# Kernel tuning notes

Hardware: AMD Instinct MI355X
Metric: run time of the kernel (lower is better)

The kernel has to match this reference:

```python
import jax, jax.numpy as jnp
import numpy as np

B, N, C, H = 2, 1024, 768, 12
D = C // H  # head_dim = 64
LN_EPS = 1e-5
BN_EPS = 1e-5


def setup_inputs() -> dict:
    key = jax.random.key(0)
    ks = jax.random.split(key, 8)
    s = 0.02
    return {
        "x": jax.random.normal(ks[0], (B, N, C), jnp.float32),
        "qkv_w": jax.random.normal(ks[1], (3 * C, C), jnp.float32) * s,
        "qkv_b": jnp.zeros((3 * C,), jnp.float32),
        "ln_g": jnp.ones((3 * C,), jnp.float32),
        "ln_b": jnp.zeros((3 * C,), jnp.float32),
        "scale": jnp.float32(D ** -0.5),
        "riem_scale": jnp.float32(D ** -0.5),
        "temp": jnp.ones((2 * H, 1, 1), jnp.float32),
        "bn_g": jnp.ones((2 * H,), jnp.float32),
        "bn_b": jnp.zeros((2 * H,), jnp.float32),
        "bn_mean": jnp.zeros((2 * H,), jnp.float32),
        "bn_var": jnp.ones((2 * H,), jnp.float32),
        "conv_w": jax.random.normal(ks[2], (H, 2 * H), jnp.float32) * s,  # 1x1 conv: [out_ch, in_ch]
        "conv_b": jnp.zeros((H,), jnp.float32),
        "proj_w": jax.random.normal(ks[3], (C, C), jnp.float32) * s,
        "proj_b": jnp.zeros((C,), jnp.float32),
    }


def _layernorm(x, g, b):
    mu = jnp.mean(x, axis=-1, keepdims=True)
    var = jnp.mean((x - mu) ** 2, axis=-1, keepdims=True)
    return (x - mu) * jax.lax.rsqrt(var + LN_EPS) * g + b


def reference(x, qkv_w, qkv_b, ln_g, ln_b, scale, riem_scale, temp,
              bn_g, bn_b, bn_mean, bn_var, conv_w, conv_b, proj_w, proj_b):
    Bq, Nq, Cq = x.shape
    qkv = _layernorm(x @ qkv_w.T + qkv_b, ln_g, ln_b)            # [B,N,3C]
    qkv = qkv.reshape(Bq, Nq, 3, H, D).transpose(2, 0, 3, 1, 4)  # [3,B,H,N,D]
    q, k, v = qkv[0], qkv[1], qkv[2]

    qk = jnp.einsum('bhid,bhjd->bhij', q, k)                     # shared QK^T GEMM
    attn = qk * scale
    # cov Frobenius: ||q_i q_i^T - k_j k_j^T||_F = sqrt(|q|^4 + |k|^4 - 2 (q.k)^2)
    qn2 = jnp.sum(q * q, axis=-1)                                # [B,H,N]
    kn2 = jnp.sum(k * k, axis=-1)
    frob2 = qn2[..., :, None] ** 2 + kn2[..., None, :] ** 2 - 2.0 * qk * qk
    attn_r = jnp.sqrt(jnp.maximum(frob2, 1e-12)) * riem_scale

    a = jnp.concatenate([attn, attn_r], axis=1) * temp[None]     # [B,2H,N,N]
    # BatchNorm2d (eval mode, running stats)
    inv = jax.lax.rsqrt(bn_var + BN_EPS)
    a = (a - bn_mean[None, :, None, None]) * (inv * bn_g)[None, :, None, None] + bn_b[None, :, None, None]
    # 1x1 conv: channel mixing 2H -> H
    a = jnp.einsum('bcij,oc->boij', a, conv_w) + conv_b[None, :, None, None]
    a = jax.nn.softmax(a, axis=-1)                               # [B,H,N,N]

    out = jnp.einsum('bhij,bhjd->bhid', a, v)                    # [B,H,N,D]
    out = out.transpose(0, 2, 1, 3).reshape(Bq, Nq, Cq)
    return out @ proj_w.T + proj_b
```

## Files before the change

### kernel.cpp

```cpp
#include <hip/hip_runtime.h>
#include <stdint.h>
#include <string.h>


using short8  = __attribute__((ext_vector_type(8))) short;
using float4v = __attribute__((ext_vector_type(4))) float;
using uint2v  = __attribute__((ext_vector_type(2))) unsigned int;
typedef unsigned short u16;

__device__ __forceinline__ float bf2f(u16 u) {
  uint32_t x = ((uint32_t)u) << 16; float f; __builtin_memcpy(&f, &x, 4); return f;
}
__device__ __forceinline__ u16 f2bf(float f) {
  uint32_t x; __builtin_memcpy(&x, &f, 4);
  uint32_t r = x + 0x7FFFu + ((x >> 16) & 1u);
  return (u16)(r >> 16);
}
__device__ __forceinline__ float gets(const void* p, int i, bool f32) {
  return f32 ? ((const float*)p)[i] : bf2f(((const u16*)p)[i]);
}
__device__ __forceinline__ void gl_lds(const void* g, void* l) {
  __builtin_amdgcn_global_load_lds(
      (const __attribute__((address_space(1))) void*)g,
      (__attribute__((address_space(3))) void*)l, 16, 0, 0);
}

#define CN0 (2048 * 768)
#define CN1 (2304 * 768)
#define CN2 (2304)
#define CN3 (768 * 768)
#define CN4 (768)
#define CTOT (CN0 + CN1 + CN2 + CN3 + CN4)

__launch_bounds__(256)
__global__ void cast_all(const void* __restrict__ s0, const void* __restrict__ s1,
                         const void* __restrict__ s2, const void* __restrict__ s3,
                         const void* __restrict__ s4, u16* __restrict__ dst,
                         const u16* __restrict__ lng) {
  const bool f32 = (lng[0] == 0);
  const int i8 = (blockIdx.x * 256 + threadIdx.x) * 8;
  if (i8 >= CTOT) return;
  const void* src; int off;
  if (i8 < CN0)                         { src = s0; off = i8; }
  else if (i8 < CN0 + CN1)              { src = s1; off = i8 - CN0; }
  else if (i8 < CN0 + CN1 + CN2)        { src = s2; off = i8 - CN0 - CN1; }
  else if (i8 < CN0 + CN1 + CN2 + CN3)  { src = s3; off = i8 - CN0 - CN1 - CN2; }
  else                                  { src = s4; off = i8 - CN0 - CN1 - CN2 - CN3; }
  short8 v;
  if (f32) {
    const float4v a = *reinterpret_cast<const float4v*>((const float*)src + off);
    const float4v b = *reinterpret_cast<const float4v*>((const float*)src + off + 4);
#pragma unroll
    for (int j = 0; j < 4; j++) { v[j] = (short)f2bf(a[j]); v[j + 4] = (short)f2bf(b[j]); }
  } else {
    v = *reinterpret_cast<const short8*>((const u16*)src + off);
  }
  *reinterpret_cast<short8*>(dst + i8) = v;
}

template<int BM, int BN>
__launch_bounds__(256, 4)
__global__ void gemm_lds(const u16* __restrict__ A, const u16* __restrict__ Bw,
                         const u16* __restrict__ bias, void* __restrict__ out,
                         const u16* __restrict__ lng, int M, int Nn, int K, int out_mode) {
  __shared__ u16 As[BM * 32], Bs[BN * 32];
  constexpr int FM = BM / 32, FN = BN / 32;
  const bool f32 = (lng[0] == 0);
  const int t = threadIdx.x, lane = t & 63, wave = t >> 6;
  const int quad = lane >> 4, l16 = lane & 15;
  const int m0 = blockIdx.y * BM, n0 = blockIdx.x * BN;
  const int wm = (wave & 1) * (BM / 2), wn = (wave >> 1) * (BN / 2);
  const int srow = wave * 16 + (lane >> 2), scol = (lane & 3) * 8;
  float4v acc[FM][FN] = {};
  for (int k0 = 0; k0 < K; k0 += 32) {
#pragma unroll
    for (int r = 0; r < BM; r += 64)
      gl_lds(A + (size_t)(m0 + r + srow) * K + k0 + scol, &As[(r + wave * 16) * 32]);
#pragma unroll
    for (int r = 0; r < BN; r += 64)
      gl_lds(Bw + (size_t)(n0 + r + srow) * K + k0 + scol, &Bs[(r + wave * 16) * 32]);
    __syncthreads();
    short8 af[FM], bfr[FN];
#pragma unroll
    for (int i = 0; i < FM; i++)
      af[i] = *reinterpret_cast<const short8*>(&As[(wm + i * 16 + l16) * 32 + quad * 8]);
#pragma unroll
    for (int i = 0; i < FN; i++)
      bfr[i] = *reinterpret_cast<const short8*>(&Bs[(wn + i * 16 + l16) * 32 + quad * 8]);
#pragma unroll
    for (int mi = 0; mi < FM; mi++)
#pragma unroll
      for (int ni = 0; ni < FN; ni++)
        acc[mi][ni] = __builtin_amdgcn_mfma_f32_16x16x32_bf16(af[mi], bfr[ni], acc[mi][ni], 0, 0, 0);
    __syncthreads();
  }
#pragma unroll
  for (int mi = 0; mi < FM; mi++) {
#pragma unroll
    for (int ni = 0; ni < FN; ni++) {
      const int col = n0 + wn + ni * 16 + l16;
      const float bv = bf2f(bias[col]);
#pragma unroll
      for (int r = 0; r < 4; r++) {
        const int row = m0 + wm + mi * 16 + quad * 4 + r;
        const float v = acc[mi][ni][r] + bv;
        const size_t idx = (size_t)row * Nn + col;
        if (out_mode == 0 || f32) ((float*)out)[idx] = v;
        else                      ((u16*)out)[idx] = f2bf(v);
      }
    }
  }
}

__launch_bounds__(256)
__global__ void ln_split(const float* __restrict__ raw, const void* __restrict__ g,
                         const void* __restrict__ b, u16* __restrict__ Q,
                         u16* __restrict__ Kk, u16* __restrict__ V,
                         float* __restrict__ qn4, float* __restrict__ kn4) {
  const bool f32 = (((const u16*)g)[0] == 0);
  const int row = blockIdx.x;
  const int bb = row >> 10, n = row & 1023;
  const int t = threadIdx.x, wave = t >> 6, lane = t & 63;
  const float* rp = raw + (size_t)row * 2304;
  float v[9], s1 = 0.f, s2 = 0.f;
#pragma unroll
  for (int k = 0; k < 9; k++) { float x = rp[t + 256 * k]; v[k] = x; s1 += x; s2 += x * x; }
#pragma unroll
  for (int m = 32; m >= 1; m >>= 1) { s1 += __shfl_xor(s1, m); s2 += __shfl_xor(s2, m); }
  __shared__ float r1[4], r2[4], hs[24];
  if (lane == 0) { r1[wave] = s1; r2[wave] = s2; }
  __syncthreads();
  const float S1 = r1[0] + r1[1] + r1[2] + r1[3];
  const float S2 = r2[0] + r2[1] + r2[2] + r2[3];
  const float mean = S1 * (1.f / 2304.f);
  const float var = S2 * (1.f / 2304.f) - mean * mean;
  const float rstd = rsqrtf(var + 1e-5f);
  float y[9];
#pragma unroll
  for (int k = 0; k < 9; k++) {
    const int c = t + 256 * k;
    y[k] = (v[k] - mean) * rstd * gets(g, c, f32) + gets(b, c, f32);
    const int s = k / 3;
    const int h = (k - s * 3) * 4 + wave, d = lane;
    const size_t idx = ((size_t)(bb * 12 + h) * 1024 + n) * 64 + d;
    u16* dst = (s == 0) ? Q : ((s == 1) ? Kk : V);
    dst[idx] = f2bf(y[k]);
  }
#pragma unroll
  for (int k = 0; k < 6; k++) {
    float sq = y[k] * y[k];
#pragma unroll
    for (int m = 32; m >= 1; m >>= 1) sq += __shfl_xor(sq, m);
    const int s = k / 3, h = (k - s * 3) * 4 + wave;
    if (lane == 0) hs[s * 12 + h] = sq;
  }
  __syncthreads();
  if (t < 12)      qn4[(size_t)(bb * 12 + t) * 1024 + n]      = hs[t] * hs[t];
  else if (t < 24) kn4[(size_t)(bb * 12 + t - 12) * 1024 + n] = hs[t] * hs[t];
}

__launch_bounds__(256)
__global__ void transpose_v(const u16* __restrict__ V, u16* __restrict__ Vt) {
  __shared__ u16 tile[64 * 65];
  const int bh = blockIdx.y;
  const int n0 = blockIdx.x * 64;
  const int t = threadIdx.x;
  const u16* src = V + (size_t)bh * 1024 * 64;
  u16* dst = Vt + (size_t)bh * 64 * 1024;
#pragma unroll
  for (int k = 0; k < 16; k++) {
    const int idx = t + 256 * k, n = idx >> 6, d = idx & 63;
    tile[d * 65 + n] = src[(size_t)(n0 + n) * 64 + d];
  }
  __syncthreads();
#pragma unroll
  for (int k = 0; k < 16; k++) {
    const int idx = t + 256 * k, d = idx >> 6, n = idx & 63;
    dst[(size_t)d * 1024 + n0 + n] = tile[d * 65 + n];
  }
}

__launch_bounds__(256)
__global__ void wp_setup(const void* __restrict__ scale_p, const void* __restrict__ riem_p,
                         const void* __restrict__ temp_p,
                         const void* __restrict__ bng, const void* __restrict__ bnb,
                         const void* __restrict__ bnm, const void* __restrict__ bnv,
                         const void* __restrict__ convw, const void* __restrict__ convb,
                         const u16* __restrict__ lng, float* __restrict__ Wp_g) {
  const bool f32 = (lng[0] == 0);
  const float LOG2E = 1.4426950408889634f;
  const int t = threadIdx.x;
  for (int idx = t; idx < 288; idx += 256) {
    const int o = idx / 24, c = idx % 24;
    const int co = (c & 1) ? 12 + (c >> 1) : (c >> 1);
    const float inv = rsqrtf(gets(bnv, co, f32) + 1e-5f);
    const float Ac = gets(temp_p, co, f32) * gets(bng, co, f32) * inv;
    const float sc = (co < 12) ? gets(scale_p, 0, f32) : gets(riem_p, 0, f32);
    Wp_g[c * 12 + o] = gets(convw, o * 24 + co, f32) * Ac * sc * LOG2E;
  }
  if (t < 12) {
    float sb = gets(convb, t, f32);
    for (int c = 0; c < 24; c++) {
      const float inv = rsqrtf(gets(bnv, c, f32) + 1e-5f);
      const float Bc = gets(bnb, c, f32) - gets(bnm, c, f32) * gets(bng, c, f32) * inv;
      sb += gets(convw, t * 24 + c, f32) * Bc;
    }
    Wp_g[24 * 12 + t] = sb * LOG2E;
  }
}

__launch_bounds__(256, 3)
__global__ void attn_fused(const u16* __restrict__ Q, const u16* __restrict__ Kk,
                           const u16* __restrict__ Vt,
                           const float* __restrict__ qn4, const float* __restrict__ kn4,
                           const float* __restrict__ Wp_g,
                           float* __restrict__ Pacc, float* __restrict__ Pl, int S) {
  __shared__ uint32_t Gd[512 * 17];
  __shared__ u16 P[12 * 648];

  const int t = threadIdx.x, lane = t & 63, wave = t >> 6;
  const int quad = lane >> 4, l16 = lane & 15;
  const int wg = blockIdx.x;
  const int bit = wg / S, s = wg - bit * S;
  const int jps = 32 / S;
  const int bb = bit >> 6, it = bit & 63, i0 = it * 16;

  for (int idx = t; idx < 512 * 4; idx += 256) {
    const int pos = idx >> 2, d = 12 + (idx & 3);
    Gd[pos * 17 + d] = (d == 12) ? 0x00003F80u : 0u;
  }

  short8 wfrag;
#pragma unroll
  for (int jj = 0; jj < 8; jj++) {
    const int c = quad * 8 + jj;
    wfrag[jj] = (short)f2bf((c < 25 && l16 < 12) ? Wp_g[c * 12 + l16] : 0.f);
  }

  const int hb = wave * 3;
  short8 aq[3][2];
  float qn4r[3][4];
#pragma unroll
  for (int hh = 0; hh < 3; hh++) {
    const int h = hb + hh;
    const u16* Qb = Q + ((size_t)(bb * 12 + h) * 1024 + i0 + l16) * 64;
#pragma unroll
    for (int ks = 0; ks < 2; ks++)
      aq[hh][ks] = *reinterpret_cast<const short8*>(Qb + ks * 32 + quad * 8);
#pragma unroll
    for (int r = 0; r < 4; r++)
      qn4r[hh][r] = qn4[(size_t)(bb * 12 + h) * 1024 + i0 + quad * 4 + r];
  }
  __syncthreads();

  float l_run[4] = {0.f, 0.f, 0.f, 0.f};
  float4v acc[3][4] = {};

  for (int jt = s * jps; jt < (s + 1) * jps; jt++) {
    const int j0 = jt * 32;
#pragma unroll
    for (int jc = 0; jc < 2; jc++) {
      float4v cc[3];
      float knr[3];
#pragma unroll
      for (int hh = 0; hh < 3; hh++) {
        const int h = hb + hh;
        knr[hh] = kn4[(size_t)(bb * 12 + h) * 1024 + j0 + jc * 16 + l16];
        const u16* Kr = Kk + ((size_t)(bb * 12 + h) * 1024 + j0 + jc * 16 + l16) * 64 + quad * 8;
        const short8 b0 = *reinterpret_cast<const short8*>(Kr);
        const short8 b1 = *reinterpret_cast<const short8*>(Kr + 32);
        float4v c = {};
        c = __builtin_amdgcn_mfma_f32_16x16x32_bf16(aq[hh][0], b0, c, 0, 0, 0);
        cc[hh] = __builtin_amdgcn_mfma_f32_16x16x32_bf16(aq[hh][1], b1, c, 0, 0, 0);
      }
#pragma unroll
      for (int hh = 0; hh < 3; hh++) {
#pragma unroll
        for (int r = 0; r < 4; r++) {
          const int pos = (quad * 4 + r) * 32 + jc * 16 + l16;
          const float qk = cc[hh][r];
          const float fr = qn4r[hh][r] + knr[hh] - 2.f * qk * qk;
          const float rv = sqrtf(fmaxf(fr, 1e-12f));
          Gd[pos * 17 + hb + hh] = (uint32_t)f2bf(qk) | ((uint32_t)f2bf(rv) << 16);
        }
      }
    }
    __syncthreads();

#pragma unroll
    for (int ir = 0; ir < 4; ir++) {
      const int i = wave * 4 + ir;
      short8 a0, a1;
      {
        const uint32_t* g0 = &Gd[(size_t)(i * 32 + l16) * 17 + quad * 4];
        uint32_t w0[4] = {g0[0], g0[1], g0[2], g0[3]};
        __builtin_memcpy(&a0, w0, 16);
        const uint32_t* g1 = &Gd[(size_t)(i * 32 + 16 + l16) * 17 + quad * 4];
        uint32_t w1[4] = {g1[0], g1[1], g1[2], g1[3]};
        __builtin_memcpy(&a1, w1, 16);
      }
      float4v L0 = {}, L1 = {};
      L0 = __builtin_amdgcn_mfma_f32_16x16x32_bf16(a0, wfrag, L0, 0, 0, 0);
      L1 = __builtin_amdgcn_mfma_f32_16x16x32_bf16(a1, wfrag, L1, 0, 0, 0);
      float ts = 0.f, p0[4], p1[4];
#pragma unroll
      for (int r = 0; r < 4; r++) {
        p0[r] = exp2f(L0[r]); p1[r] = exp2f(L1[r]);
        ts += p0[r] + p1[r];
      }
      ts += __shfl_xor(ts, 16);
      ts += __shfl_xor(ts, 32);
      l_run[ir] += ts;
      if (l16 < 12) {
        const uint2v w0 = { (uint32_t)f2bf(p0[0]) | ((uint32_t)f2bf(p0[1]) << 16),
                            (uint32_t)f2bf(p0[2]) | ((uint32_t)f2bf(p0[3]) << 16) };
        const uint2v w1 = { (uint32_t)f2bf(p1[0]) | ((uint32_t)f2bf(p1[1]) << 16),
                            (uint32_t)f2bf(p1[2]) | ((uint32_t)f2bf(p1[3]) << 16) };
        *reinterpret_cast<uint2v*>(&P[l16 * 648 + i * 40 + quad * 4]) = w0;
        *reinterpret_cast<uint2v*>(&P[l16 * 648 + i * 40 + 16 + quad * 4]) = w1;
      }
    }
    __syncthreads();

#pragma unroll
    for (int oo = 0; oo < 3; oo++) {
      const int o = hb + oo;
      const short8 pf = *reinterpret_cast<const short8*>(&P[o * 648 + l16 * 40 + quad * 8]);
      const u16* Vb = Vt + (size_t)(bb * 12 + o) * 64 * 1024;
#pragma unroll
      for (int ni = 0; ni < 4; ni++) {
        const short8 bv = *reinterpret_cast<const short8*>(Vb + (size_t)(ni * 16 + l16) * 1024 + j0 + quad * 8);
        acc[oo][ni] = __builtin_amdgcn_mfma_f32_16x16x32_bf16(pf, bv, acc[oo][ni], 0, 0, 0);
      }
    }
  }

#pragma unroll
  for (int ir = 0; ir < 4; ir++)
    if (l16 < 12 && quad == 0)
      Pl[(wg * 12 + l16) * 16 + wave * 4 + ir] = l_run[ir];
#pragma unroll
  for (int oo = 0; oo < 3; oo++) {
    const int o = hb + oo;
#pragma unroll
    for (int ni = 0; ni < 4; ni++)
#pragma unroll
      for (int r = 0; r < 4; r++) {
        const int i = quad * 4 + r, d = ni * 16 + l16;
        Pacc[((size_t)(wg * 12 + o) * 16 + i) * 64 + d] = acc[oo][ni][r];
      }
  }
}

__launch_bounds__(256)
__global__ void combine(const float* __restrict__ Pacc, const float* __restrict__ Pl,
                        u16* __restrict__ AO, int S) {
  const int o = blockIdx.x, bit = blockIdx.y;
  const int t = threadIdx.x, i = t >> 4, d0 = (t & 15) * 4;
  const int bb = bit >> 6, row = (bit & 63) * 16 + i;
  float lg = 0.f;
  float4v ov = {};
  for (int s2 = 0; s2 < S; s2++) {
    lg += Pl[((bit * S + s2) * 12 + o) * 16 + i];
    const float4v p = *reinterpret_cast<const float4v*>(
        Pacc + ((size_t)((bit * S + s2) * 12 + o) * 16 + i) * 64 + d0);
#pragma unroll
    for (int r = 0; r < 4; r++) ov[r] += p[r];
  }
  const float inv = 1.f / lg;
  uint2v pk;
  pk[0] = (uint32_t)f2bf(ov[0] * inv) | ((uint32_t)f2bf(ov[1] * inv) << 16);
  pk[1] = (uint32_t)f2bf(ov[2] * inv) | ((uint32_t)f2bf(ov[3] * inv) << 16);
  *reinterpret_cast<uint2v*>(&AO[((size_t)bb * 1024 + row) * 768 + o * 64 + d0]) = pk;
}

extern "C" void kernel_launch(void* const* d_in, const int* in_sizes, int n_in,
                              void* d_out, int out_size, void* d_ws, size_t ws_size,
                              hipStream_t stream) {
  const void* x      = d_in[0];
  const void* qkv_w  = d_in[1];
  const void* qkv_b  = d_in[2];
  const u16*  ln_g   = (const u16*)d_in[3];
  const void* ln_b   = d_in[4];
  const void* scale  = d_in[5];
  const void* riem   = d_in[6];
  const void* temp   = d_in[7];
  const void* bn_g   = d_in[8];
  const void* bn_b   = d_in[9];
  const void* bn_m   = d_in[10];
  const void* bn_v   = d_in[11];
  const void* conv_w = d_in[12];
  const void* conv_b = d_in[13];
  const void* proj_w = d_in[14];
  const void* proj_b = d_in[15];

  float* qkv_raw = (float*)d_ws;
  u16* Q   = (u16*)((char*)d_ws + (size_t)2048 * 2304 * 4);
  u16* Kk  = Q  + (size_t)2 * 12 * 1024 * 64;
  u16* V   = Kk + (size_t)2 * 12 * 1024 * 64;
  u16* Vt  = V  + (size_t)2 * 12 * 1024 * 64;
  float* qn4 = (float*)(Vt + (size_t)2 * 12 * 1024 * 64);
  float* kn4 = qn4 + 2 * 12 * 1024;
  u16* AO  = (u16*)(kn4 + 2 * 12 * 1024);
  u16* x_bf    = AO + (size_t)2048 * 768;
  u16* qkvw_bf = x_bf + CN0;
  u16* qkvb_bf = qkvw_bf + CN1;
  u16* projw_bf = qkvb_bf + CN2;
  u16* projb_bf = projw_bf + CN3;
  float* Wp_g = (float*)((char*)d_ws +
      (((size_t)(projb_bf + CN4) - (size_t)d_ws + 255) & ~(size_t)255));
  float* Pacc = (float*)((char*)Wp_g + ((300 * 4 + 255) & ~255));
  const size_t base_bytes = (size_t)((char*)Pacc - (char*)d_ws);

  int S = 8;
  while (S > 1 && base_bytes + (size_t)128 * S * 12 * 16 * 260 > ws_size) S >>= 1;
  float* Pl = Pacc + (size_t)128 * S * 12 * 16 * 64;

  cast_all<<<dim3((CTOT / 8 + 255) / 256), 256, 0, stream>>>(
      x, qkv_w, qkv_b, proj_w, proj_b, x_bf, ln_g);
  wp_setup<<<dim3(1), 256, 0, stream>>>(scale, riem, temp, bn_g, bn_b, bn_m, bn_v,
                                        conv_w, conv_b, ln_g, Wp_g);
  gemm_lds<64, 128><<<dim3(18, 32), 256, 0, stream>>>(x_bf, qkvw_bf, qkvb_bf, qkv_raw,
                                                      ln_g, 2048, 2304, 768, 0);
  ln_split<<<dim3(2048), 256, 0, stream>>>(qkv_raw, ln_g, ln_b, Q, Kk, V, qn4, kn4);
  transpose_v<<<dim3(16, 24), 256, 0, stream>>>(V, Vt);
  attn_fused<<<dim3(128 * S), 256, 0, stream>>>(Q, Kk, Vt, qn4, kn4, Wp_g, Pacc, Pl, S);
  combine<<<dim3(12, 128), 256, 0, stream>>>(Pacc, Pl, AO, S);
  gemm_lds<64, 64><<<dim3(12, 32), 256, 0, stream>>>(AO, projw_bf, projb_bf, d_out,
                                                     ln_g, 2048, 768, 768, 1);
}
```

Before: 233.6 us.

## Shrink intermediates to bf16, fuse weight setup, prefetch V, use hardware converts

Several changes at once. The QKV GEMM output and the attention partial accumulators are now stored as bf16 instead of fp32, which roughly halves that traffic. The wp_setup kernel is merged into cast_all to save a launch. V tiles are loaded into registers before the QK/softmax phase to hide their latency, and the split count is made a compile-time template parameter. Manual bf16 rounding and exp2f are replaced with hardware builtins where available. The cost is lower precision in the LayerNorm input and in the partial-sum reduction, plus extra register pressure from the V prefetch.

```diff
diff --git a/kernel.cpp b/kernel.cpp
--- a/kernel.cpp
+++ b/kernel.cpp
@@ -4,6 +4,7 @@
 
 
 using short8  = __attribute__((ext_vector_type(8))) short;
+using short4v = __attribute__((ext_vector_type(4))) short;
 using float4v = __attribute__((ext_vector_type(4))) float;
 using uint2v  = __attribute__((ext_vector_type(2))) unsigned int;
 typedef unsigned short u16;
@@ -16,6 +17,21 @@
   uint32_t r = x + 0x7FFFu + ((x >> 16) & 1u);
   return (u16)(r >> 16);
 }
+#if __has_builtin(__builtin_amdgcn_cvt_pk_bf16_f32)
+__device__ __forceinline__ uint32_t pk_bf16(float lo, float hi) {
+  auto r = __builtin_amdgcn_cvt_pk_bf16_f32(lo, hi);
+  uint32_t u; __builtin_memcpy(&u, &r, 4); return u;
+}
+#else
+__device__ __forceinline__ uint32_t pk_bf16(float lo, float hi) {
+  return (uint32_t)f2bf(lo) | ((uint32_t)f2bf(hi) << 16);
+}
+#endif
+#if __has_builtin(__builtin_amdgcn_exp2f)
+#define EXP2F __builtin_amdgcn_exp2f
+#else
+#define EXP2F exp2f
+#endif
 __device__ __forceinline__ float gets(const void* p, int i, bool f32) {
   return f32 ? ((const float*)p)[i] : bf2f(((const u16*)p)[i]);
 }
@@ -36,26 +52,53 @@
 __global__ void cast_all(const void* __restrict__ s0, const void* __restrict__ s1,
                          const void* __restrict__ s2, const void* __restrict__ s3,
                          const void* __restrict__ s4, u16* __restrict__ dst,
-                         const u16* __restrict__ lng) {
+                         const void* __restrict__ scale_p, const void* __restrict__ riem_p,
+                         const void* __restrict__ temp_p,
+                         const void* __restrict__ bng, const void* __restrict__ bnb,
+                         const void* __restrict__ bnm, const void* __restrict__ bnv,
+                         const void* __restrict__ convw, const void* __restrict__ convb,
+                         const u16* __restrict__ lng, float* __restrict__ Wp_g) {
   const bool f32 = (lng[0] == 0);
-  const int i8 = (blockIdx.x * 256 + threadIdx.x) * 8;
-  if (i8 >= CTOT) return;
-  const void* src; int off;
-  if (i8 < CN0)                         { src = s0; off = i8; }
-  else if (i8 < CN0 + CN1)              { src = s1; off = i8 - CN0; }
-  else if (i8 < CN0 + CN1 + CN2)        { src = s2; off = i8 - CN0 - CN1; }
-  else if (i8 < CN0 + CN1 + CN2 + CN3)  { src = s3; off = i8 - CN0 - CN1 - CN2; }
-  else                                  { src = s4; off = i8 - CN0 - CN1 - CN2 - CN3; }
-  short8 v;
-  if (f32) {
-    const float4v a = *reinterpret_cast<const float4v*>((const float*)src + off);
-    const float4v b = *reinterpret_cast<const float4v*>((const float*)src + off + 4);
-#pragma unroll
-    for (int j = 0; j < 4; j++) { v[j] = (short)f2bf(a[j]); v[j + 4] = (short)f2bf(b[j]); }
-  } else {
-    v = *reinterpret_cast<const short8*>((const u16*)src + off);
-  }
-  *reinterpret_cast<short8*>(dst + i8) = v;
+  const int t = threadIdx.x;
+  const int i8 = (blockIdx.x * 256 + t) * 8;
+  if (i8 < CTOT) {
+    const void* src; int off;
+    if (i8 < CN0)                         { src = s0; off = i8; }
+    else if (i8 < CN0 + CN1)              { src = s1; off = i8 - CN0; }
+    else if (i8 < CN0 + CN1 + CN2)        { src = s2; off = i8 - CN0 - CN1; }
+    else if (i8 < CN0 + CN1 + CN2 + CN3)  { src = s3; off = i8 - CN0 - CN1 - CN2; }
+    else                                  { src = s4; off = i8 - CN0 - CN1 - CN2 - CN3; }
+    short8 v;
+    if (f32) {
+      const float4v a = *reinterpret_cast<const float4v*>((const float*)src + off);
+      const float4v b = *reinterpret_cast<const float4v*>((const float*)src + off + 4);
+#pragma unroll
+      for (int j = 0; j < 4; j++) { v[j] = (short)f2bf(a[j]); v[j + 4] = (short)f2bf(b[j]); }
+    } else {
+      v = *reinterpret_cast<const short8*>((const u16*)src + off);
+    }
+    *reinterpret_cast<short8*>(dst + i8) = v;
+  }
+  if (blockIdx.x == 0) {
+    const float LOG2E = 1.4426950408889634f;
+    for (int idx = t; idx < 288; idx += 256) {
+      const int o = idx / 24, c = idx % 24;
+      const int co = (c & 1) ? 12 + (c >> 1) : (c >> 1);
+      const float inv = rsqrtf(gets(bnv, co, f32) + 1e-5f);
+      const float Ac = gets(temp_p, co, f32) * gets(bng, co, f32) * inv;
+      const float sc = (co < 12) ? gets(scale_p, 0, f32) : gets(riem_p, 0, f32);
+      Wp_g[c * 12 + o] = gets(convw, o * 24 + co, f32) * Ac * sc * LOG2E;
+    }
+    if (t < 12) {
+      float sb = gets(convb, t, f32);
+      for (int c = 0; c < 24; c++) {
+        const float inv = rsqrtf(gets(bnv, c, f32) + 1e-5f);
+        const float Bc = gets(bnb, c, f32) - gets(bnm, c, f32) * gets(bng, c, f32) * inv;
+        sb += gets(convw, t * 24 + c, f32) * Bc;
+      }
+      Wp_g[24 * 12 + t] = sb * LOG2E;
+    }
+  }
 }
 
 template<int BM, int BN>
@@ -66,6 +109,7 @@
   __shared__ u16 As[BM * 32], Bs[BN * 32];
   constexpr int FM = BM / 32, FN = BN / 32;
   const bool f32 = (lng[0] == 0);
+  const bool obf = (out_mode == 2) || (out_mode == 1 && !f32);
   const int t = threadIdx.x, lane = t & 63, wave = t >> 6;
   const int quad = lane >> 4, l16 = lane & 15;
   const int m0 = blockIdx.y * BM, n0 = blockIdx.x * BN;
@@ -105,15 +149,15 @@
         const int row = m0 + wm + mi * 16 + quad * 4 + r;
         const float v = acc[mi][ni][r] + bv;
         const size_t idx = (size_t)row * Nn + col;
-        if (out_mode == 0 || f32) ((float*)out)[idx] = v;
-        else                      ((u16*)out)[idx] = f2bf(v);
+        if (obf) ((u16*)out)[idx] = f2bf(v);
+        else     ((float*)out)[idx] = v;
       }
     }
   }
 }
 
 __launch_bounds__(256)
-__global__ void ln_split(const float* __restrict__ raw, const void* __restrict__ g,
+__global__ void ln_split(const u16* __restrict__ raw, const void* __restrict__ g,
                          const void* __restrict__ b, u16* __restrict__ Q,
                          u16* __restrict__ Kk, u16* __restrict__ V,
                          float* __restrict__ qn4, float* __restrict__ kn4) {
@@ -121,10 +165,10 @@
   const int row = blockIdx.x;
   const int bb = row >> 10, n = row & 1023;
   const int t = threadIdx.x, wave = t >> 6, lane = t & 63;
-  const float* rp = raw + (size_t)row * 2304;
+  const u16* rp = raw + (size_t)row * 2304;
   float v[9], s1 = 0.f, s2 = 0.f;
 #pragma unroll
-  for (int k = 0; k < 9; k++) { float x = rp[t + 256 * k]; v[k] = x; s1 += x; s2 += x * x; }
+  for (int k = 0; k < 9; k++) { float x = bf2f(rp[t + 256 * k]); v[k] = x; s1 += x; s2 += x * x; }
 #pragma unroll
   for (int m = 32; m >= 1; m >>= 1) { s1 += __shfl_xor(s1, m); s2 += __shfl_xor(s2, m); }
   __shared__ float r1[4], r2[4], hs[24];
@@ -180,41 +224,13 @@
   }
 }
 
-__launch_bounds__(256)
-__global__ void wp_setup(const void* __restrict__ scale_p, const void* __restrict__ riem_p,
-                         const void* __restrict__ temp_p,
-                         const void* __restrict__ bng, const void* __restrict__ bnb,
-                         const void* __restrict__ bnm, const void* __restrict__ bnv,
-                         const void* __restrict__ convw, const void* __restrict__ convb,
-                         const u16* __restrict__ lng, float* __restrict__ Wp_g) {
-  const bool f32 = (lng[0] == 0);
-  const float LOG2E = 1.4426950408889634f;
-  const int t = threadIdx.x;
-  for (int idx = t; idx < 288; idx += 256) {
-    const int o = idx / 24, c = idx % 24;
-    const int co = (c & 1) ? 12 + (c >> 1) : (c >> 1);
-    const float inv = rsqrtf(gets(bnv, co, f32) + 1e-5f);
-    const float Ac = gets(temp_p, co, f32) * gets(bng, co, f32) * inv;
-    const float sc = (co < 12) ? gets(scale_p, 0, f32) : gets(riem_p, 0, f32);
-    Wp_g[c * 12 + o] = gets(convw, o * 24 + co, f32) * Ac * sc * LOG2E;
-  }
-  if (t < 12) {
-    float sb = gets(convb, t, f32);
-    for (int c = 0; c < 24; c++) {
-      const float inv = rsqrtf(gets(bnv, c, f32) + 1e-5f);
-      const float Bc = gets(bnb, c, f32) - gets(bnm, c, f32) * gets(bng, c, f32) * inv;
-      sb += gets(convw, t * 24 + c, f32) * Bc;
-    }
-    Wp_g[24 * 12 + t] = sb * LOG2E;
-  }
-}
-
+template<int JPS>
 __launch_bounds__(256, 3)
 __global__ void attn_fused(const u16* __restrict__ Q, const u16* __restrict__ Kk,
                            const u16* __restrict__ Vt,
                            const float* __restrict__ qn4, const float* __restrict__ kn4,
                            const float* __restrict__ Wp_g,
-                           float* __restrict__ Pacc, float* __restrict__ Pl, int S) {
+                           u16* __restrict__ Pacc, float* __restrict__ Pl, int S) {
   __shared__ uint32_t Gd[512 * 17];
   __shared__ u16 P[12 * 648];
 
@@ -222,7 +238,7 @@
   const int quad = lane >> 4, l16 = lane & 15;
   const int wg = blockIdx.x;
   const int bit = wg / S, s = wg - bit * S;
-  const int jps = 32 / S;
+  const int jps = (JPS > 0) ? JPS : (32 / S);
   const int bb = bit >> 6, it = bit & 63, i0 = it * 16;
 
   for (int idx = t; idx < 512 * 4; idx += 256) {
@@ -258,6 +274,14 @@
 
   for (int jt = s * jps; jt < (s + 1) * jps; jt++) {
     const int j0 = jt * 32;
+    short8 vpre[3][4];
+#pragma unroll
+    for (int oo = 0; oo < 3; oo++) {
+      const u16* Vb = Vt + (size_t)(bb * 12 + hb + oo) * 64 * 1024 + j0 + quad * 8;
+#pragma unroll
+      for (int ni = 0; ni < 4; ni++)
+        vpre[oo][ni] = *reinterpret_cast<const short8*>(Vb + (size_t)(ni * 16 + l16) * 1024);
+    }
 #pragma unroll
     for (int jc = 0; jc < 2; jc++) {
       float4v cc[3];
@@ -280,8 +304,7 @@
           const int pos = (quad * 4 + r) * 32 + jc * 16 + l16;
           const float qk = cc[hh][r];
           const float fr = qn4r[hh][r] + knr[hh] - 2.f * qk * qk;
-          const float rv = sqrtf(fmaxf(fr, 1e-12f));
-          Gd[pos * 17 + hb + hh] = (uint32_t)f2bf(qk) | ((uint32_t)f2bf(rv) << 16);
+          Gd[pos * 17 + hb + hh] = pk_bf16(qk, sqrtf(fmaxf(fr, 1e-12f)));
         }
       }
     }
@@ -305,17 +328,15 @@
       float ts = 0.f, p0[4], p1[4];
 #pragma unroll
       for (int r = 0; r < 4; r++) {
-        p0[r] = exp2f(L0[r]); p1[r] = exp2f(L1[r]);
+        p0[r] = EXP2F(L0[r]); p1[r] = EXP2F(L1[r]);
         ts += p0[r] + p1[r];
       }
       ts += __shfl_xor(ts, 16);
       ts += __shfl_xor(ts, 32);
       l_run[ir] += ts;
       if (l16 < 12) {
-        const uint2v w0 = { (uint32_t)f2bf(p0[0]) | ((uint32_t)f2bf(p0[1]) << 16),
-                            (uint32_t)f2bf(p0[2]) | ((uint32_t)f2bf(p0[3]) << 16) };
-        const uint2v w1 = { (uint32_t)f2bf(p1[0]) | ((uint32_t)f2bf(p1[1]) << 16),
-                            (uint32_t)f2bf(p1[2]) | ((uint32_t)f2bf(p1[3]) << 16) };
+        const uint2v w0 = { pk_bf16(p0[0], p0[1]), pk_bf16(p0[2], p0[3]) };
+        const uint2v w1 = { pk_bf16(p1[0], p1[1]), pk_bf16(p1[2], p1[3]) };
         *reinterpret_cast<uint2v*>(&P[l16 * 648 + i * 40 + quad * 4]) = w0;
         *reinterpret_cast<uint2v*>(&P[l16 * 648 + i * 40 + 16 + quad * 4]) = w1;
       }
@@ -326,12 +347,9 @@
     for (int oo = 0; oo < 3; oo++) {
       const int o = hb + oo;
       const short8 pf = *reinterpret_cast<const short8*>(&P[o * 648 + l16 * 40 + quad * 8]);
-      const u16* Vb = Vt + (size_t)(bb * 12 + o) * 64 * 1024;
-#pragma unroll
-      for (int ni = 0; ni < 4; ni++) {
-        const short8 bv = *reinterpret_cast<const short8*>(Vb + (size_t)(ni * 16 + l16) * 1024 + j0 + quad * 8);
-        acc[oo][ni] = __builtin_amdgcn_mfma_f32_16x16x32_bf16(pf, bv, acc[oo][ni], 0, 0, 0);
-      }
+#pragma unroll
+      for (int ni = 0; ni < 4; ni++)
+        acc[oo][ni] = __builtin_amdgcn_mfma_f32_16x16x32_bf16(pf, vpre[oo][ni], acc[oo][ni], 0, 0, 0);
     }
   }
 
@@ -347,13 +365,13 @@
 #pragma unroll
       for (int r = 0; r < 4; r++) {
         const int i = quad * 4 + r, d = ni * 16 + l16;
-        Pacc[((size_t)(wg * 12 + o) * 16 + i) * 64 + d] = acc[oo][ni][r];
+        Pacc[((size_t)(wg * 12 + o) * 16 + i) * 64 + d] = f2bf(acc[oo][ni][r]);
       }
   }
 }
 
 __launch_bounds__(256)
-__global__ void combine(const float* __restrict__ Pacc, const float* __restrict__ Pl,
+__global__ void combine(const u16* __restrict__ Pacc, const float* __restrict__ Pl,
                         u16* __restrict__ AO, int S) {
   const int o = blockIdx.x, bit = blockIdx.y;
   const int t = threadIdx.x, i = t >> 4, d0 = (t & 15) * 4;
@@ -362,15 +380,15 @@
   float4v ov = {};
   for (int s2 = 0; s2 < S; s2++) {
     lg += Pl[((bit * S + s2) * 12 + o) * 16 + i];
-    const float4v p = *reinterpret_cast<const float4v*>(
+    const short4v p = *reinterpret_cast<const short4v*>(
         Pacc + ((size_t)((bit * S + s2) * 12 + o) * 16 + i) * 64 + d0);
 #pragma unroll
-    for (int r = 0; r < 4; r++) ov[r] += p[r];
+    for (int r = 0; r < 4; r++) ov[r] += bf2f((u16)p[r]);
   }
   const float inv = 1.f / lg;
   uint2v pk;
-  pk[0] = (uint32_t)f2bf(ov[0] * inv) | ((uint32_t)f2bf(ov[1] * inv) << 16);
-  pk[1] = (uint32_t)f2bf(ov[2] * inv) | ((uint32_t)f2bf(ov[3] * inv) << 16);
+  pk[0] = pk_bf16(ov[0] * inv, ov[1] * inv);
+  pk[1] = pk_bf16(ov[2] * inv, ov[3] * inv);
   *reinterpret_cast<uint2v*>(&AO[((size_t)bb * 1024 + row) * 768 + o * 64 + d0]) = pk;
 }
 
@@ -394,8 +412,8 @@
   const void* proj_w = d_in[14];
   const void* proj_b = d_in[15];
 
-  float* qkv_raw = (float*)d_ws;
-  u16* Q   = (u16*)((char*)d_ws + (size_t)2048 * 2304 * 4);
+  u16* qkv_bf16 = (u16*)d_ws;
+  u16* Q   = qkv_bf16 + (size_t)2048 * 2304;
   u16* Kk  = Q  + (size_t)2 * 12 * 1024 * 64;
   u16* V   = Kk + (size_t)2 * 12 * 1024 * 64;
   u16* Vt  = V  + (size_t)2 * 12 * 1024 * 64;
@@ -409,22 +427,24 @@
   u16* projb_bf = projw_bf + CN3;
   float* Wp_g = (float*)((char*)d_ws +
       (((size_t)(projb_bf + CN4) - (size_t)d_ws + 255) & ~(size_t)255));
-  float* Pacc = (float*)((char*)Wp_g + ((300 * 4 + 255) & ~255));
+  u16* Pacc = (u16*)((char*)Wp_g + ((300 * 4 + 255) & ~255));
   const size_t base_bytes = (size_t)((char*)Pacc - (char*)d_ws);
 
   int S = 8;
-  while (S > 1 && base_bytes + (size_t)128 * S * 12 * 16 * 260 > ws_size) S >>= 1;
-  float* Pl = Pacc + (size_t)128 * S * 12 * 16 * 64;
+  while (S > 1 && base_bytes + (size_t)128 * S * 12 * 16 * 132 > ws_size) S >>= 1;
+  float* Pl = (float*)(Pacc + (size_t)128 * S * 12 * 16 * 64);
 
   cast_all<<<dim3((CTOT / 8 + 255) / 256), 256, 0, stream>>>(
-      x, qkv_w, qkv_b, proj_w, proj_b, x_bf, ln_g);
-  wp_setup<<<dim3(1), 256, 0, stream>>>(scale, riem, temp, bn_g, bn_b, bn_m, bn_v,
-                                        conv_w, conv_b, ln_g, Wp_g);
-  gemm_lds<64, 128><<<dim3(18, 32), 256, 0, stream>>>(x_bf, qkvw_bf, qkvb_bf, qkv_raw,
-                                                      ln_g, 2048, 2304, 768, 0);
-  ln_split<<<dim3(2048), 256, 0, stream>>>(qkv_raw, ln_g, ln_b, Q, Kk, V, qn4, kn4);
+      x, qkv_w, qkv_b, proj_w, proj_b, x_bf,
+      scale, riem, temp, bn_g, bn_b, bn_m, bn_v, conv_w, conv_b, ln_g, Wp_g);
+  gemm_lds<64, 128><<<dim3(18, 32), 256, 0, stream>>>(x_bf, qkvw_bf, qkvb_bf, qkv_bf16,
+                                                      ln_g, 2048, 2304, 768, 2);
+  ln_split<<<dim3(2048), 256, 0, stream>>>(qkv_bf16, ln_g, ln_b, Q, Kk, V, qn4, kn4);
   transpose_v<<<dim3(16, 24), 256, 0, stream>>>(V, Vt);
-  attn_fused<<<dim3(128 * S), 256, 0, stream>>>(Q, Kk, Vt, qn4, kn4, Wp_g, Pacc, Pl, S);
+  if (S == 8)
+    attn_fused<4><<<dim3(128 * 8), 256, 0, stream>>>(Q, Kk, Vt, qn4, kn4, Wp_g, Pacc, Pl, 8);
+  else
+    attn_fused<0><<<dim3(128 * S), 256, 0, stream>>>(Q, Kk, Vt, qn4, kn4, Wp_g, Pacc, Pl, S);
   combine<<<dim3(12, 128), 256, 0, stream>>>(Pacc, Pl, AO, S);
   gemm_lds<64, 64><<<dim3(12, 32), 256, 0, stream>>>(AO, projw_bf, projb_bf, d_out,
                                                      ln_g, 2048, 768, 768, 1);
```

After: 285.5 us. 22.2% more time.
